# Performance work log

Measured on AMD Instinct MI355X. Metric: run time of the kernel, lower is better.

The kernel has to match this reference:

```python
import jax, jax.numpy as jnp
import numpy as np

EPS = 1e-6
HEADS = 8

def _ln_cf(x, w, b):
    # ConvNeXt-style channels_first LayerNorm over C axis of (B,C,H,W)
    mu = jnp.mean(x, axis=1, keepdims=True)
    var = jnp.mean((x - mu) ** 2, axis=1, keepdims=True)
    xn = (x - mu) / jnp.sqrt(var + EPS)
    return xn * w[None, :, None, None] + b[None, :, None, None]

def _xattn(q_map, kv_map, Wq, Wk, Wv, Wo, bo):
    B, C, H, W = q_map.shape
    HW = H * W
    dh = C // HEADS
    xq = q_map.reshape(B, C, HW).transpose(0, 2, 1)   # (B,HW,C)
    xkv = kv_map.reshape(B, C, HW).transpose(0, 2, 1)
    q = (xq @ Wq.T).reshape(B, HW, HEADS, dh).transpose(0, 2, 1, 3)
    k = (xkv @ Wk.T).reshape(B, HW, HEADS, dh).transpose(0, 2, 1, 3)
    v = (xkv @ Wv.T).reshape(B, HW, HEADS, dh).transpose(0, 2, 1, 3)
    scale = dh ** -0.5
    logits = jnp.einsum('bhqd,bhkd->bhqk', q, k) * scale
    attn = jax.nn.softmax(logits, axis=-1)
    o = jnp.einsum('bhqk,bhkd->bhqd', attn, v)        # (B,h,HW,dh)
    o = o.transpose(0, 2, 1, 3).reshape(B, HW, C)
    o = o @ Wo.T + bo
    return o.transpose(0, 2, 1).reshape(B, C, H, W)

def _ffn(x, W1, b1, W2, b2):
    # 1x1 convs == channel-wise linear; exact GELU (torch default)
    h = jnp.einsum('bchw,oc->bohw', x, W1) + b1[None, :, None, None]
    h = jax.nn.gelu(h, approximate=False)
    return jnp.einsum('bchw,oc->bohw', h, W2) + b2[None, :, None, None]

def setup_inputs() -> dict:
    key = jax.random.key(0)
    ks = jax.random.split(key, 24)
    B, C, H, W = 8, 512, 32, 32
    hid = 4 * C
    d = {
        'spatial_feat': jax.random.normal(ks[0], (B, C, H, W), jnp.float32),
        'freq_feat': jax.random.normal(ks[1], (B, C, H, W), jnp.float32),
        # spatial enhancer (standard cross-attn)
        's_Wq': jax.random.normal(ks[2], (C, C), jnp.float32) * 0.02,
        's_Wk': jax.random.normal(ks[3], (C, C), jnp.float32) * 0.02,
        's_Wv': jax.random.normal(ks[4], (C, C), jnp.float32) * 0.02,
        's_Wo': jax.random.normal(ks[5], (C, C), jnp.float32) * 0.02,
        's_bo': jnp.zeros((C,), jnp.float32),
        # frequency enhancer
        'f_Wq': jax.random.normal(ks[6], (C, C), jnp.float32) * 0.02,
        'f_Wk': jax.random.normal(ks[7], (C, C), jnp.float32) * 0.02,
        'f_Wv': jax.random.normal(ks[8], (C, C), jnp.float32) * 0.02,
        'f_Wo': jax.random.normal(ks[9], (C, C), jnp.float32) * 0.02,
        'f_bo': jnp.zeros((C,), jnp.float32),
        # norms
        'sn1_w': jnp.ones((C,), jnp.float32), 'sn1_b': jnp.zeros((C,), jnp.float32),
        'sn2_w': jnp.ones((C,), jnp.float32), 'sn2_b': jnp.zeros((C,), jnp.float32),
        'fn1_w': jnp.ones((C,), jnp.float32), 'fn1_b': jnp.zeros((C,), jnp.float32),
        'fn2_w': jnp.ones((C,), jnp.float32), 'fn2_b': jnp.zeros((C,), jnp.float32),
        # ConvFFNs (1x1 convs)
        'sffn_W1': jax.random.normal(ks[10], (hid, C), jnp.float32) * 0.02,
        'sffn_b1': jnp.zeros((hid,), jnp.float32),
        'sffn_W2': jax.random.normal(ks[11], (C, hid), jnp.float32) * 0.02,
        'sffn_b2': jnp.zeros((C,), jnp.float32),
        'fffn_W1': jax.random.normal(ks[12], (hid, C), jnp.float32) * 0.02,
        'fffn_b1': jnp.zeros((hid,), jnp.float32),
        'fffn_W2': jax.random.normal(ks[13], (C, hid), jnp.float32) * 0.02,
        'fffn_b2': jnp.zeros((C,), jnp.float32),
    }
    return d

def reference(spatial_feat, freq_feat,
              s_Wq, s_Wk, s_Wv, s_Wo, s_bo,
              f_Wq, f_Wk, f_Wv, f_Wo, f_bo,
              sn1_w, sn1_b, sn2_w, sn2_b,
              fn1_w, fn1_b, fn2_w, fn2_b,
              sffn_W1, sffn_b1, sffn_W2, sffn_b2,
              fffn_W1, fffn_b1, fffn_W2, fffn_b2):
    enh_s = _xattn(spatial_feat, freq_feat, s_Wq, s_Wk, s_Wv, s_Wo, s_bo)
    enh_f = _xattn(freq_feat, spatial_feat, f_Wq, f_Wk, f_Wv, f_Wo, f_bo)
    s = _ln_cf(spatial_feat + enh_s, sn1_w, sn1_b)
    s = _ln_cf(s + _ffn(s, sffn_W1, sffn_b1, sffn_W2, sffn_b2), sn2_w, sn2_b)
    f = _ln_cf(freq_feat + enh_f, fn1_w, fn1_b)
    f = _ln_cf(f + _ffn(f, fffn_W1, fffn_b1, fffn_W2, fffn_b2), fn2_w, fn2_b)
    return (s, f)
```

## Files before the change

### kernel.cpp

```cpp
#include <hip/hip_runtime.h>
#include <hip/hip_bf16.h>


#define CCH 512
#define HWD 1024

typedef unsigned short u16;
typedef unsigned int u32;
typedef __attribute__((ext_vector_type(8))) __bf16 bf16x8;
typedef __attribute__((ext_vector_type(4))) float f32x4;
typedef __attribute__((ext_vector_type(4))) unsigned short u16x4;
typedef __attribute__((ext_vector_type(8))) unsigned short u16x8;

__device__ __forceinline__ float bf2f(u16 u) { return __uint_as_float(((u32)u) << 16); }
__device__ __forceinline__ u16 f2bf(float f) {
    u32 u = __float_as_uint(f);
    return (u16)((u + 0x7fffu + ((u >> 16) & 1u)) >> 16);
}
__device__ __forceinline__ float ldp(const void* p, int i, bool isbf) {
    return isbf ? bf2f(((const u16*)p)[i]) : ((const float*)p)[i];
}
__device__ __forceinline__ float fast_gelu(float v) {
    float a = v * (0.7978845608f + 0.0356774081f * v * v);
    float e = __expf(-2.0f * fabsf(a));
    float r = __fdividef(1.0f - e, 1.0f + e);
    float th = (a < 0.f) ? -r : r;
    return 0.5f * v * (1.0f + th);
}

#define GLL16(g, l) __builtin_amdgcn_global_load_lds( \
    (const __attribute__((address_space(1))) u32*)(g), \
    (__attribute__((address_space(3))) u32*)(l), 16, 0, 0)

struct MMJob { const u16* A; const u16* W; const void* bias; void* Y; };
struct PJob  { const u16* A; const u16* W; u16* Y; int ldY; int gm; int gn; };
struct PJobs { PJob j[6]; };
struct AJob  { const u16* QK; const u16* VT; u16* AO; };
struct LNJob { const u16* A; const float* Br; const void* w; const void* b; void* Y; };

__global__ void k_detect(const u16* __restrict__ in, int* __restrict__ flag) {
    if (threadIdx.x == 0 && blockIdx.x == 0) {
        int sane = 0;
        for (int i = 0; i < 1024; i += 2) {
            int e = (in[i] >> 7) & 0xFF;
            if (e >= 0x6D && e <= 0x8D) sane++;
        }
        *flag = (sane >= 256) ? 1 : 0;
    }
}

struct CvtJobs {
    const void* src[12];
    u16* dst[12];
    int chunk0[13];
};
__global__ __launch_bounds__(256) void k_cvt_all(CvtJobs J, const int* __restrict__ flag) {
    bool isbf = (*flag != 0);
    int b = blockIdx.x;
    int j = 0;
    #pragma unroll
    for (int i = 0; i < 12; i++) if (b >= J.chunk0[i + 1]) j = i + 1;
    int idx = (b - J.chunk0[j]) * 1024 + threadIdx.x * 4;
    u16* d = J.dst[j] + idx;
    if (isbf) {
        *(u16x4*)d = *(const u16x4*)((const u16*)J.src[j] + idx);
    } else {
        float4 v = *(const float4*)((const float*)J.src[j] + idx);
        d[0] = f2bf(v.x); d[1] = f2bf(v.y); d[2] = f2bf(v.z); d[3] = f2bf(v.w);
    }
}

__global__ __launch_bounds__(256) void k_transpose(const void* __restrict__ in,
                                                   u16* __restrict__ out,
                                                   const int* __restrict__ flag) {
    __shared__ float tile[32][33];
    bool isbf = (*flag != 0);
    int b = blockIdx.z;
    int hw0 = blockIdx.x * 32, c0 = blockIdx.y * 32;
    int tx = threadIdx.x, ty = threadIdx.y;
    size_t base = (size_t)b * CCH * HWD;
    if (isbf) {
        const u16* ip = (const u16*)in + base;
        for (int i = ty; i < 32; i += 8)
            tile[i][tx] = bf2f(ip[(size_t)(c0 + i) * HWD + hw0 + tx]);
    } else {
        const float* ip = (const float*)in + base;
        for (int i = ty; i < 32; i += 8)
            tile[i][tx] = ip[(size_t)(c0 + i) * HWD + hw0 + tx];
    }
    __syncthreads();
    u16* op = out + (size_t)b * HWD * CCH;
    for (int i = ty; i < 32; i += 8)
        op[(size_t)(hw0 + i) * CCH + c0 + tx] = f2bf(tile[tx][i]);
}

__device__ __forceinline__ void swz(int pid, int gm, int gn, int& bm, int& bn) {
    int gsz = 8 * gn;
    int gid = pid / gsz;
    int fm = gid * 8;
    int rows = (gm - fm < 8) ? (gm - fm) : 8;
    int pin = pid - gid * gsz;
    bm = fm + pin % rows;
    bn = pin / rows;
}

__global__ __launch_bounds__(256) void k_mm(MMJob j0, MMJob j1,
                                            int K, int ldY, int mode, int gm, int gn,
                                            const int* __restrict__ flag) {
    __shared__ u16 As[128 * 32];
    __shared__ u16 Bs[128 * 32];
    MMJob J = blockIdx.z ? j1 : j0;
    int t = threadIdx.x;
    int w = t >> 6, l = t & 63;
    int bm, bn;
    swz(blockIdx.x, gm, gn, bm, bn);
    int m0 = bm * 128, n0 = bn * 128;
    int wm = (w >> 1) * 64, wn = (w & 1) * 64;

    int r0 = (w * 2 + 0) * 16 + (l >> 2);
    int r1 = (w * 2 + 1) * 16 + (l >> 2);
    int sg0 = (((l & 3) ^ ((r0 >> 1) & 3))) * 8;
    int sg1 = (((l & 3) ^ ((r1 >> 1) & 3))) * 8;
    const u16* ga0 = J.A + (size_t)(m0 + r0) * K + sg0;
    const u16* ga1 = J.A + (size_t)(m0 + r1) * K + sg1;
    const u16* gb0 = J.W + (size_t)(n0 + r0) * K + sg0;
    const u16* gb1 = J.W + (size_t)(n0 + r1) * K + sg1;
    u16* la0 = &As[(w * 2 + 0) * 512];
    u16* la1 = &As[(w * 2 + 1) * 512];
    u16* lb0 = &Bs[(w * 2 + 0) * 512];
    u16* lb1 = &Bs[(w * 2 + 1) * 512];

    int quad = l >> 4, lr = l & 15;
    int aoff[4], boff[4];
    #pragma unroll
    for (int i = 0; i < 4; i++) {
        int ra = wm + i * 16 + lr, rb = wn + i * 16 + lr;
        aoff[i] = ra * 32 + (quad ^ ((ra >> 1) & 3)) * 8;
        boff[i] = rb * 32 + (quad ^ ((rb >> 1) & 3)) * 8;
    }

    f32x4 acc[4][4] = {};

    for (int k0 = 0; k0 < K; k0 += 32) {
        __syncthreads();
        GLL16(ga0 + k0, la0);
        GLL16(ga1 + k0, la1);
        GLL16(gb0 + k0, lb0);
        GLL16(gb1 + k0, lb1);
        __syncthreads();
        bf16x8 af[4], bfr[4];
        #pragma unroll
        for (int i = 0; i < 4; i++) af[i] = *(const bf16x8*)&As[aoff[i]];
        #pragma unroll
        for (int j = 0; j < 4; j++) bfr[j] = *(const bf16x8*)&Bs[boff[j]];
        #pragma unroll
        for (int i = 0; i < 4; i++)
            #pragma unroll
            for (int j = 0; j < 4; j++)
                acc[i][j] = __builtin_amdgcn_mfma_f32_16x16x32_bf16(af[i], bfr[j], acc[i][j], 0, 0, 0);
    }

    bool isbf = (*flag != 0);
    #pragma unroll
    for (int i = 0; i < 4; i++) {
        int rowb = m0 + wm + i * 16 + quad * 4;
        #pragma unroll
        for (int j = 0; j < 4; j++) {
            int col = n0 + wn + j * 16 + lr;
            float bv = (mode == 1 || mode == 2) ? ldp(J.bias, col, isbf) : 0.f;
            #pragma unroll
            for (int r = 0; r < 4; r++) {
                float v = acc[i][j][r] + bv;
                if (mode == 2) {
                    ((u16*)J.Y)[(size_t)(rowb + r) * ldY + col] = f2bf(fast_gelu(v));
                } else if (mode == 3) {
                    ((u16*)J.Y)[(size_t)(rowb + r) * ldY + col] = f2bf(v);
                } else {
                    ((float*)J.Y)[(size_t)(rowb + r) * ldY + col] = v;
                }
            }
        }
    }
}

__global__ __launch_bounds__(256) void k_mm64(MMJob j0, MMJob j1,
                                              int K, int ldY, int mode, int gm, int gn,
                                              const int* __restrict__ flag) {
    __shared__ u16 As[128 * 32];
    __shared__ u16 Bs[64 * 32];
    MMJob J = blockIdx.z ? j1 : j0;
    int t = threadIdx.x;
    int w = t >> 6, l = t & 63;
    int bm, bn;
    swz(blockIdx.x, gm, gn, bm, bn);
    int m0 = bm * 128, n0 = bn * 64;
    int wm = (w >> 1) * 64, wn = (w & 1) * 32;

    int r0 = (w * 2 + 0) * 16 + (l >> 2);
    int r1 = (w * 2 + 1) * 16 + (l >> 2);
    int rb_ = w * 16 + (l >> 2);
    int sg0 = (((l & 3) ^ ((r0 >> 1) & 3))) * 8;
    int sg1 = (((l & 3) ^ ((r1 >> 1) & 3))) * 8;
    int sgb = (((l & 3) ^ ((rb_ >> 1) & 3))) * 8;
    const u16* ga0 = J.A + (size_t)(m0 + r0) * K + sg0;
    const u16* ga1 = J.A + (size_t)(m0 + r1) * K + sg1;
    const u16* gb  = J.W + (size_t)(n0 + rb_) * K + sgb;
    u16* la0 = &As[(w * 2 + 0) * 512];
    u16* la1 = &As[(w * 2 + 1) * 512];
    u16* lb  = &Bs[w * 512];

    int quad = l >> 4, lr = l & 15;
    int aoff[4], boff[2];
    #pragma unroll
    for (int i = 0; i < 4; i++) {
        int ra = wm + i * 16 + lr;
        aoff[i] = ra * 32 + (quad ^ ((ra >> 1) & 3)) * 8;
    }
    #pragma unroll
    for (int j = 0; j < 2; j++) {
        int rb2 = wn + j * 16 + lr;
        boff[j] = rb2 * 32 + (quad ^ ((rb2 >> 1) & 3)) * 8;
    }

    f32x4 acc[4][2] = {};

    for (int k0 = 0; k0 < K; k0 += 32) {
        __syncthreads();
        GLL16(ga0 + k0, la0);
        GLL16(ga1 + k0, la1);
        GLL16(gb + k0, lb);
        __syncthreads();
        bf16x8 af[4], bfr[2];
        #pragma unroll
        for (int i = 0; i < 4; i++) af[i] = *(const bf16x8*)&As[aoff[i]];
        #pragma unroll
        for (int j = 0; j < 2; j++) bfr[j] = *(const bf16x8*)&Bs[boff[j]];
        #pragma unroll
        for (int i = 0; i < 4; i++)
            #pragma unroll
            for (int j = 0; j < 2; j++)
                acc[i][j] = __builtin_amdgcn_mfma_f32_16x16x32_bf16(af[i], bfr[j], acc[i][j], 0, 0, 0);
    }

    bool isbf = (*flag != 0);
    #pragma unroll
    for (int i = 0; i < 4; i++) {
        int rowb = m0 + wm + i * 16 + quad * 4;
        #pragma unroll
        for (int j = 0; j < 2; j++) {
            int col = n0 + wn + j * 16 + lr;
            float bv = (mode == 1 || mode == 2) ? ldp(J.bias, col, isbf) : 0.f;
            #pragma unroll
            for (int r = 0; r < 4; r++) {
                float v = acc[i][j][r] + bv;
                if (mode == 2) {
                    ((u16*)J.Y)[(size_t)(rowb + r) * ldY + col] = f2bf(fast_gelu(v));
                } else if (mode == 3) {
                    ((u16*)J.Y)[(size_t)(rowb + r) * ldY + col] = f2bf(v);
                } else {
                    ((float*)J.Y)[(size_t)(rowb + r) * ldY + col] = v;
                }
            }
        }
    }
}

__global__ __launch_bounds__(256) void k_proj(PJobs JJ, const int* __restrict__ flag) {
    __shared__ u16 As[128 * 32];
    __shared__ u16 Bs[64 * 32];
    (void)flag;
    PJob J = JJ.j[blockIdx.z];
    const int K = 512;
    int t = threadIdx.x;
    int w = t >> 6, l = t & 63;
    int bm, bn;
    swz(blockIdx.x, J.gm, J.gn, bm, bn);
    int m0 = bm * 128, n0 = bn * 64;
    int wm = (w >> 1) * 64, wn = (w & 1) * 32;

    int r0 = (w * 2 + 0) * 16 + (l >> 2);
    int r1 = (w * 2 + 1) * 16 + (l >> 2);
    int rb_ = w * 16 + (l >> 2);
    int sg0 = (((l & 3) ^ ((r0 >> 1) & 3))) * 8;
    int sg1 = (((l & 3) ^ ((r1 >> 1) & 3))) * 8;
    int sgb = (((l & 3) ^ ((rb_ >> 1) & 3))) * 8;
    const u16* ga0 = J.A + (size_t)(m0 + r0) * K + sg0;
    const u16* ga1 = J.A + (size_t)(m0 + r1) * K + sg1;
    const u16* gb  = J.W + (size_t)(n0 + rb_) * K + sgb;
    u16* la0 = &As[(w * 2 + 0) * 512];
    u16* la1 = &As[(w * 2 + 1) * 512];
    u16* lb  = &Bs[w * 512];

    int quad = l >> 4, lr = l & 15;
    int aoff[4], boff[2];
    #pragma unroll
    for (int i = 0; i < 4; i++) {
        int ra = wm + i * 16 + lr;
        aoff[i] = ra * 32 + (quad ^ ((ra >> 1) & 3)) * 8;
    }
    #pragma unroll
    for (int j = 0; j < 2; j++) {
        int rb2 = wn + j * 16 + lr;
        boff[j] = rb2 * 32 + (quad ^ ((rb2 >> 1) & 3)) * 8;
    }

    f32x4 acc[4][2] = {};

    for (int k0 = 0; k0 < K; k0 += 32) {
        __syncthreads();
        GLL16(ga0 + k0, la0);
        GLL16(ga1 + k0, la1);
        GLL16(gb + k0, lb);
        __syncthreads();
        bf16x8 af[4], bfr[2];
        #pragma unroll
        for (int i = 0; i < 4; i++) af[i] = *(const bf16x8*)&As[aoff[i]];
        #pragma unroll
        for (int j = 0; j < 2; j++) bfr[j] = *(const bf16x8*)&Bs[boff[j]];
        #pragma unroll
        for (int i = 0; i < 4; i++)
            #pragma unroll
            for (int j = 0; j < 2; j++)
                acc[i][j] = __builtin_amdgcn_mfma_f32_16x16x32_bf16(af[i], bfr[j], acc[i][j], 0, 0, 0);
    }

    #pragma unroll
    for (int i = 0; i < 4; i++) {
        int rowb = m0 + wm + i * 16 + quad * 4;
        #pragma unroll
        for (int j = 0; j < 2; j++) {
            int col = n0 + wn + j * 16 + lr;
            #pragma unroll
            for (int r = 0; r < 4; r++)
                J.Y[(size_t)(rowb + r) * J.ldY + col] = f2bf(acc[i][j][r]);
        }
    }
}

__global__ __launch_bounds__(256) void k_attn2(AJob j0, AJob j1) {
    __shared__ __align__(16) u16 Qs[2][128][32];
    __shared__ __align__(16) u16 Ks[2][64][32];
    __shared__ __align__(16) u16 Vs[2][64][32];
    __shared__ __align__(16) u16 Ps[4][32][80];

    AJob J = (blockIdx.x >> 9) ? j1 : j0;
    int blk = blockIdx.x & 511;
    int t = threadIdx.x;
    int w = t >> 6, l = t & 63;
    int l15 = l & 15, quad = l >> 4;
    int qt = blk & 7;
    int bh = blk >> 3;
    int h = bh & 7, b = bh >> 3;
    int tok0 = b * 1024;
    int q0 = qt * 128;
    int hc = h * 64;

    #pragma unroll
    for (int kc = 0; kc < 2; kc++)
        #pragma unroll
        for (int g = 0; g < 2; g++) {
            int row = w * 32 + g * 16 + (l >> 2);
            int sl = ((l & 3) ^ ((row >> 1) & 3)) * 8;
            const u16* gp = J.QK + (size_t)(tok0 + q0 + row) * 1024 + hc + kc * 32 + sl;
            GLL16(gp, &Qs[kc][w * 32 + g * 16][0]);
        }
    __syncthreads();

    bf16x8 qf[2][2];
    #pragma unroll
    for (int jq = 0; jq < 2; jq++)
        #pragma unroll
        for (int kc = 0; kc < 2; kc++) {
            int row = w * 32 + jq * 16 + l15;
            qf[jq][kc] = *(const bf16x8*)&Qs[kc][row][(quad ^ ((row >> 1) & 3)) * 8];
        }

    float m_[2] = {-1e30f, -1e30f};
    float l_[2] = {0.f, 0.f};
    f32x4 acco[2][4] = {};

    for (int kt = 0; kt < 16; kt++) {
        __syncthreads();
        {
            int row = w * 16 + (l >> 2);
            int f = (row >> 1) & 3;
            int sl = ((l & 3) ^ f) * 8;
            int key = kt * 64 + row;
            #pragma unroll
            for (int kc = 0; kc < 2; kc++) {
                const u16* kp = J.QK + (size_t)(tok0 + key) * 1024 + 512 + hc + kc * 32 + sl;
                GLL16(kp, &Ks[kc][w * 16][0]);
            }
            #pragma unroll
            for (int kck = 0; kck < 2; kck++) {
                const u16* vp = J.VT + (size_t)(hc + row) * 8192 + tok0 + kt * 64 + kck * 32 + sl;
                GLL16(vp, &Vs[kck][w * 16][0]);
            }
        }
        __syncthreads();

        f32x4 accs[4][2] = {};
        #pragma unroll
        for (int kc = 0; kc < 2; kc++) {
            bf16x8 kf[4];
            #pragma unroll
            for (int i = 0; i < 4; i++) {
                int row = i * 16 + l15;
                kf[i] = *(const bf16x8*)&Ks[kc][row][(quad ^ ((row >> 1) & 3)) * 8];
            }
            #pragma unroll
            for (int i = 0; i < 4; i++)
                #pragma unroll
                for (int jq = 0; jq < 2; jq++)
                    accs[i][jq] = __builtin_amdgcn_mfma_f32_16x16x32_bf16(kf[i], qf[jq][kc], accs[i][jq], 0, 0, 0);
        }

        float alpha[2];
        #pragma unroll
        for (int jq = 0; jq < 2; jq++) {
            float tm = -1e30f;
            #pragma unroll
            for (int i = 0; i < 4; i++)
                #pragma unroll
                for (int r = 0; r < 4; r++) tm = fmaxf(tm, accs[i][jq][r]);
            tm *= 0.125f;
            tm = fmaxf(tm, __shfl_xor(tm, 16));
            tm = fmaxf(tm, __shfl_xor(tm, 32));
            float mn = fmaxf(m_[jq], tm);
            alpha[jq] = __expf(m_[jq] - mn);
            m_[jq] = mn;
            float ts = 0.f;
            #pragma unroll
            for (int i = 0; i < 4; i++) {
                u16x4 pk;
                #pragma unroll
                for (int r = 0; r < 4; r++) {
                    float p = __expf(accs[i][jq][r] * 0.125f - mn);
                    ts += p;
                    pk[r] = f2bf(p);
                }
                *(u16x4*)&Ps[w][jq * 16 + l15][i * 16 + quad * 4] = pk;
            }
            ts += __shfl_xor(ts, 16);
            ts += __shfl_xor(ts, 32);
            l_[jq] = l_[jq] * alpha[jq] + ts;
        }

        #pragma unroll
        for (int i2 = 0; i2 < 2; i2++)
            #pragma unroll
            for (int r = 0; r < 4; r++) {
                float al = __shfl(alpha[i2], quad * 4 + r);
                #pragma unroll
                for (int jd = 0; jd < 4; jd++) acco[i2][jd][r] *= al;
            }

        #pragma unroll
        for (int kck = 0; kck < 2; kck++) {
            bf16x8 pf[2], vf[4];
            #pragma unroll
            for (int i2 = 0; i2 < 2; i2++)
                pf[i2] = *(const bf16x8*)&Ps[w][i2 * 16 + l15][kck * 32 + quad * 8];
            #pragma unroll
            for (int jd = 0; jd < 4; jd++) {
                int row = jd * 16 + l15;
                vf[jd] = *(const bf16x8*)&Vs[kck][row][(quad ^ ((row >> 1) & 3)) * 8];
            }
            #pragma unroll
            for (int i2 = 0; i2 < 2; i2++)
                #pragma unroll
                for (int jd = 0; jd < 4; jd++)
                    acco[i2][jd] = __builtin_amdgcn_mfma_f32_16x16x32_bf16(pf[i2], vf[jd], acco[i2][jd], 0, 0, 0);
        }
    }

    #pragma unroll
    for (int i2 = 0; i2 < 2; i2++) {
        float linv = 1.0f / l_[i2];
        #pragma unroll
        for (int r = 0; r < 4; r++) {
            float li = __shfl(linv, quad * 4 + r);
            int token = tok0 + q0 + w * 32 + i2 * 16 + quad * 4 + r;
            u16* dst = J.AO + (size_t)token * 512 + hc;
            #pragma unroll
            for (int jd = 0; jd < 4; jd++)
                dst[jd * 16 + l15] = f2bf(acco[i2][jd][r] * li);
        }
    }
}

__global__ __launch_bounds__(256) void k_ln(LNJob j0, LNJob j1,
                                            const int* __restrict__ flag) {
    LNJob J = blockIdx.y ? j1 : j0;
    bool isbf = (*flag != 0);
    int token = blockIdx.x * 4 + (threadIdx.x >> 6);
    int lane = threadIdx.x & 63;
    int c0 = lane * 8;
    const u16* pa = J.A + (size_t)token * CCH + c0;
    const float* pb = J.Br + (size_t)token * CCH + c0;
    u16x8 av = *(const u16x8*)pa;
    float4 b0 = *(const float4*)pb;
    float4 b1 = *(const float4*)(pb + 4);
    float v[8];
    float s = 0.f, s2 = 0.f;
    #pragma unroll
    for (int u = 0; u < 8; u++) {
        float x = bf2f(av[u]) + ((u < 4) ? (&b0.x)[u] : (&b1.x)[u - 4]);
        v[u] = x; s += x; s2 += x * x;
    }
    #pragma unroll
    for (int off = 32; off > 0; off >>= 1) {
        s += __shfl_xor(s, off);
        s2 += __shfl_xor(s2, off);
    }
    float mu = s * (1.f / CCH);
    float var = s2 * (1.f / CCH) - mu * mu;
    float rstd = rsqrtf(var + 1e-6f);
    u16x8 ov;
    #pragma unroll
    for (int u = 0; u < 8; u++)
        ov[u] = f2bf((v[u] - mu) * rstd * ldp(J.w, c0 + u, isbf) + ldp(J.b, c0 + u, isbf));
    *(u16x8*)((u16*)J.Y + (size_t)token * CCH + c0) = ov;
}

__global__ __launch_bounds__(256) void k_ln_out(LNJob j0, LNJob j1,
                                                void* __restrict__ out, int brBase,
                                                const int* __restrict__ flag) {
    LNJob J = blockIdx.y ? j1 : j0;
    int branch = brBase + blockIdx.y;
    bool isbf = (*flag != 0);
    int token = blockIdx.x * 4 + (threadIdx.x >> 6);
    int lane = threadIdx.x & 63;
    int c0 = lane * 8;
    const u16* pa = J.A + (size_t)token * CCH + c0;
    const float* pb = J.Br + (size_t)token * CCH + c0;
    u16x8 av = *(const u16x8*)pa;
    float4 b0 = *(const float4*)pb;
    float4 b1 = *(const float4*)(pb + 4);
    float v[8];
    float s = 0.f, s2 = 0.f;
    #pragma unroll
    for (int u = 0; u < 8; u++) {
        float x = bf2f(av[u]) + ((u < 4) ? (&b0.x)[u] : (&b1.x)[u - 4]);
        v[u] = x; s += x; s2 += x * x;
    }
    #pragma unroll
    for (int off = 32; off > 0; off >>= 1) {
        s += __shfl_xor(s, off);
        s2 += __shfl_xor(s2, off);
    }
    float mu = s * (1.f / CCH);
    float var = s2 * (1.f / CCH) - mu * mu;
    float rstd = rsqrtf(var + 1e-6f);
    int b = token >> 10, hw = token & 1023;
    size_t obase = (size_t)branch * CCH * HWD * 8 + (size_t)b * CCH * HWD + hw;
    if (isbf) {
        u16* op = (u16*)out + obase;
        #pragma unroll
        for (int u = 0; u < 8; u++) {
            float y = (v[u] - mu) * rstd * ldp(J.w, c0 + u, true) + ldp(J.b, c0 + u, true);
            op[(size_t)(c0 + u) * HWD] = f2bf(y);
        }
    } else {
        float* op = (float*)out + obase;
        #pragma unroll
        for (int u = 0; u < 8; u++) {
            float y = (v[u] - mu) * rstd * ldp(J.w, c0 + u, false) + ldp(J.b, c0 + u, false);
            op[(size_t)(c0 + u) * HWD] = y;
        }
    }
}

extern "C" void kernel_launch(void* const* d_in, const int* in_sizes, int n_in,
                              void* d_out, int out_size, void* d_ws, size_t ws_size,
                              hipStream_t stream) {
    (void)in_sizes; (void)n_in; (void)out_size;

    char* wsb = (char*)d_ws;
    int* flag = (int*)wsb;
    u16* Wall = (u16*)(wsb + 256);
    u16* Xs = (u16*)(wsb + 256 + 12582912);
    u16* Xf = (u16*)(wsb + 256 + 12582912 + 8388608);
    char* rbase = wsb + 29360384;

    const size_t BRSZ = 67108864;
    bool dual = ws_size >= (29360384 + 2 * BRSZ);

    u16* QKb[2]; u16* VTb[2]; u16* AOb[2]; u16* Hbb[2];
    float* ENHb[2];
    for (int b = 0; b < 2; b++) {
        char* r = rbase + (dual ? b * BRSZ : 0);
        QKb[b] = (u16*)r;
        ENHb[b] = (float*)r;
        VTb[b] = (u16*)(r + 16777216);
        AOb[b] = (u16*)(r + 16777216 + 8388608);
        Hbb[b] = (u16*)(r + 16777216 + 2 * 8388608);
    }

    const int SQ = 262144, SW1 = 1048576;
    const u16* Xq[2] = {Xs, Xf};
    const u16* Xkv[2] = {Xf, Xs};
    u16* Wq[2]; u16* Wk[2]; u16* Wv[2]; u16* Wo[2]; u16* W1[2]; u16* W2[2];
    const void *bo[2], *n1w[2], *n1b[2], *n2w[2], *n2b[2], *b1[2], *b2[2];
    for (int b = 0; b < 2; b++) {
        u16* Wb = Wall + (size_t)b * 3145728;
        Wq[b] = Wb; Wk[b] = Wb + SQ; Wv[b] = Wb + 2 * SQ; Wo[b] = Wb + 3 * SQ;
        W1[b] = Wb + 4 * SQ; W2[b] = Wb + 4 * SQ + SW1;
        bo[b]  = d_in[b ? 11 : 6];
        n1w[b] = d_in[b ? 16 : 12]; n1b[b] = d_in[b ? 17 : 13];
        n2w[b] = d_in[b ? 18 : 14]; n2b[b] = d_in[b ? 19 : 15];
        b1[b]  = d_in[b ? 25 : 21]; b2[b]  = d_in[b ? 27 : 23];
    }

    k_detect<<<1, 64, 0, stream>>>((const u16*)d_in[0], flag);

    {
        CvtJobs J;
        int ch = 0;
        for (int b = 0; b < 2; b++) {
            const int srcIdx[6] = {b ? 7 : 2, b ? 8 : 3, b ? 9 : 4, b ? 10 : 5,
                                   b ? 24 : 20, b ? 26 : 22};
            u16* dsts[6] = {Wq[b], Wk[b], Wv[b], Wo[b], W1[b], W2[b]};
            const int sz[6] = {SQ, SQ, SQ, SQ, SW1, SW1};
            for (int i = 0; i < 6; i++) {
                int j = b * 6 + i;
                J.src[j] = d_in[srcIdx[i]];
                J.dst[j] = dsts[i];
                J.chunk0[j] = ch;
                ch += sz[i] / 1024;
            }
        }
        J.chunk0[12] = ch;
        k_cvt_all<<<ch, 256, 0, stream>>>(J, flag);
    }

    dim3 tb(32, 8);
    k_transpose<<<dim3(32, 16, 8), tb, 0, stream>>>(d_in[0], Xs, flag);
    k_transpose<<<dim3(32, 16, 8), tb, 0, stream>>>(d_in[1], Xf, flag);

    auto mmj = [&](const u16* A, const u16* W, const void* bias, void* Y) {
        MMJob j; j.A = A; j.W = W; j.bias = bias; j.Y = Y; return j;
    };
    auto pj = [&](const u16* A, const u16* W, u16* Y, int ldY, int gm, int gn) {
        PJob j; j.A = A; j.W = W; j.Y = Y; j.ldY = ldY; j.gm = gm; j.gn = gn; return j;
    };
    auto lnj = [&](const u16* A, const float* Br, const void* w, const void* bb, void* Y) {
        LNJob j; j.A = A; j.Br = Br; j.w = w; j.b = bb; j.Y = Y; return j;
    };

    int nbr = dual ? 2 : 1;
    int nloop = dual ? 1 : 2;
    for (int it = 0; it < nloop; it++) {
        int b0 = dual ? 0 : it;
        int b1i = dual ? 1 : it;

        {
            PJobs JJ;
            int nz = 0;
            for (int z = 0; z < nbr; z++) {
                int b = dual ? z : it;
                JJ.j[nz++] = pj(Xq[b], Wq[b], QKb[b], 1024, 64, 8);
                JJ.j[nz++] = pj(Xkv[b], Wk[b], QKb[b] + 512, 1024, 64, 8);
                JJ.j[nz++] = pj(Wv[b], Xkv[b], VTb[b], 8192, 4, 128);
            }
            for (int z = nz; z < 6; z++) JJ.j[z] = JJ.j[0];
            k_proj<<<dim3(512, 1, nz), 256, 0, stream>>>(JJ, flag);
        }
        {
            AJob a0, a1;
            a0.QK = QKb[b0]; a0.VT = VTb[b0]; a0.AO = AOb[b0];
            a1.QK = QKb[b1i]; a1.VT = VTb[b1i]; a1.AO = AOb[b1i];
            k_attn2<<<512 * nbr, 256, 0, stream>>>(a0, a1);
        }
        k_mm64<<<dim3(512, 1, nbr), 256, 0, stream>>>(
            mmj(AOb[b0], Wo[b0], bo[b0], ENHb[b0]),
            mmj(AOb[b1i], Wo[b1i], bo[b1i], ENHb[b1i]),
            512, 512, 1, 64, 8, flag);
        k_ln<<<dim3(2048, nbr), 256, 0, stream>>>(
            lnj(Xq[b0], ENHb[b0], n1w[b0], n1b[b0], AOb[b0]),
            lnj(Xq[b1i], ENHb[b1i], n1w[b1i], n1b[b1i], AOb[b1i]), flag);
        k_mm<<<dim3(1024, 1, nbr), 256, 0, stream>>>(
            mmj(AOb[b0], W1[b0], b1[b0], Hbb[b0]),
            mmj(AOb[b1i], W1[b1i], b1[b1i], Hbb[b1i]),
            512, 2048, 2, 64, 16, flag);
        k_mm64<<<dim3(512, 1, nbr), 256, 0, stream>>>(
            mmj(Hbb[b0], W2[b0], b2[b0], ENHb[b0]),
            mmj(Hbb[b1i], W2[b1i], b2[b1i], ENHb[b1i]),
            2048, 512, 1, 64, 8, flag);
        k_ln_out<<<dim3(2048, nbr), 256, 0, stream>>>(
            lnj(AOb[b0], ENHb[b0], n2w[b0], n2b[b0], nullptr),
            lnj(AOb[b1i], ENHb[b1i], n2w[b1i], n2b[b1i], nullptr),
            d_out, dual ? 0 : it, flag);
    }
}
```

Baseline: 553.2 us.

## Use sigmoid GELU, merge input transposes, and double K-step per GEMM barrier

Swaps the tanh-form GELU for a sigmoid-based x*sigmoid(1.702x) approximation, merges the two input transpose launches into one grid, and makes the three GEMM kernels load two 32-wide K slices per barrier pair. The wider K step halves the number of __syncthreads and issues more loads in flight, at the cost of doubled LDS per block and possible lower occupancy. The sigmoid GELU departs further from the exact erf GELU the reference requires, so it risks accuracy.

Result: faster. 537.0 us (-2.9%).

```diff
diff --git a/kernel.cpp b/kernel.cpp
--- a/kernel.cpp
+++ b/kernel.cpp
@@ -21,11 +21,7 @@
     return isbf ? bf2f(((const u16*)p)[i]) : ((const float*)p)[i];
 }
 __device__ __forceinline__ float fast_gelu(float v) {
-    float a = v * (0.7978845608f + 0.0356774081f * v * v);
-    float e = __expf(-2.0f * fabsf(a));
-    float r = __fdividef(1.0f - e, 1.0f + e);
-    float th = (a < 0.f) ? -r : r;
-    return 0.5f * v * (1.0f + th);
+    return v * __frcp_rn(1.0f + __expf(-1.702f * v));
 }
 
 #define GLL16(g, l) __builtin_amdgcn_global_load_lds( \
@@ -70,12 +66,17 @@
     }
 }
 
-__global__ __launch_bounds__(256) void k_transpose(const void* __restrict__ in,
-                                                   u16* __restrict__ out,
-                                                   const int* __restrict__ flag) {
+__global__ __launch_bounds__(256) void k_transpose2(const void* __restrict__ in0,
+                                                    const void* __restrict__ in1,
+                                                    u16* __restrict__ o0,
+                                                    u16* __restrict__ o1,
+                                                    const int* __restrict__ flag) {
     __shared__ float tile[32][33];
     bool isbf = (*flag != 0);
-    int b = blockIdx.z;
+    int z = blockIdx.z;
+    const void* in = (z < 8) ? in0 : in1;
+    u16* out = (z < 8) ? o0 : o1;
+    int b = z & 7;
     int hw0 = blockIdx.x * 32, c0 = blockIdx.y * 32;
     int tx = threadIdx.x, ty = threadIdx.y;
     size_t base = (size_t)b * CCH * HWD;
@@ -107,8 +108,8 @@
 __global__ __launch_bounds__(256) void k_mm(MMJob j0, MMJob j1,
                                             int K, int ldY, int mode, int gm, int gn,
                                             const int* __restrict__ flag) {
-    __shared__ u16 As[128 * 32];
-    __shared__ u16 Bs[128 * 32];
+    __shared__ u16 As[128 * 32], Asb[128 * 32];
+    __shared__ u16 Bs[128 * 32], Bsb[128 * 32];
     MMJob J = blockIdx.z ? j1 : j0;
     int t = threadIdx.x;
     int w = t >> 6, l = t & 63;
@@ -125,10 +126,7 @@
     const u16* ga1 = J.A + (size_t)(m0 + r1) * K + sg1;
     const u16* gb0 = J.W + (size_t)(n0 + r0) * K + sg0;
     const u16* gb1 = J.W + (size_t)(n0 + r1) * K + sg1;
-    u16* la0 = &As[(w * 2 + 0) * 512];
-    u16* la1 = &As[(w * 2 + 1) * 512];
-    u16* lb0 = &Bs[(w * 2 + 0) * 512];
-    u16* lb1 = &Bs[(w * 2 + 1) * 512];
+    int lo0 = (w * 2 + 0) * 512, lo1 = (w * 2 + 1) * 512;
 
     int quad = l >> 4, lr = l & 15;
     int aoff[4], boff[4];
@@ -141,23 +139,41 @@
 
     f32x4 acc[4][4] = {};
 
-    for (int k0 = 0; k0 < K; k0 += 32) {
+    for (int k0 = 0; k0 < K; k0 += 64) {
         __syncthreads();
-        GLL16(ga0 + k0, la0);
-        GLL16(ga1 + k0, la1);
-        GLL16(gb0 + k0, lb0);
-        GLL16(gb1 + k0, lb1);
+        GLL16(ga0 + k0, &As[lo0]);
+        GLL16(ga1 + k0, &As[lo1]);
+        GLL16(gb0 + k0, &Bs[lo0]);
+        GLL16(gb1 + k0, &Bs[lo1]);
+        GLL16(ga0 + k0 + 32, &Asb[lo0]);
+        GLL16(ga1 + k0 + 32, &Asb[lo1]);
+        GLL16(gb0 + k0 + 32, &Bsb[lo0]);
+        GLL16(gb1 + k0 + 32, &Bsb[lo1]);
         __syncthreads();
-        bf16x8 af[4], bfr[4];
-        #pragma unroll
-        for (int i = 0; i < 4; i++) af[i] = *(const bf16x8*)&As[aoff[i]];
-        #pragma unroll
-        for (int j = 0; j < 4; j++) bfr[j] = *(const bf16x8*)&Bs[boff[j]];
-        #pragma unroll
-        for (int i = 0; i < 4; i++)
-            #pragma unroll
-            for (int j = 0; j < 4; j++)
-                acc[i][j] = __builtin_amdgcn_mfma_f32_16x16x32_bf16(af[i], bfr[j], acc[i][j], 0, 0, 0);
+        {
+            bf16x8 af[4], bfr[4];
+            #pragma unroll
+            for (int i = 0; i < 4; i++) af[i] = *(const bf16x8*)&As[aoff[i]];
+            #pragma unroll
+            for (int j = 0; j < 4; j++) bfr[j] = *(const bf16x8*)&Bs[boff[j]];
+            #pragma unroll
+            for (int i = 0; i < 4; i++)
+                #pragma unroll
+                for (int j = 0; j < 4; j++)
+                    acc[i][j] = __builtin_amdgcn_mfma_f32_16x16x32_bf16(af[i], bfr[j], acc[i][j], 0, 0, 0);
+        }
+        {
+            bf16x8 af[4], bfr[4];
+            #pragma unroll
+            for (int i = 0; i < 4; i++) af[i] = *(const bf16x8*)&Asb[aoff[i]];
+            #pragma unroll
+            for (int j = 0; j < 4; j++) bfr[j] = *(const bf16x8*)&Bsb[boff[j]];
+            #pragma unroll
+            for (int i = 0; i < 4; i++)
+                #pragma unroll
+                for (int j = 0; j < 4; j++)
+                    acc[i][j] = __builtin_amdgcn_mfma_f32_16x16x32_bf16(af[i], bfr[j], acc[i][j], 0, 0, 0);
+        }
     }
 
     bool isbf = (*flag != 0);
@@ -186,8 +202,8 @@
 __global__ __launch_bounds__(256) void k_mm64(MMJob j0, MMJob j1,
                                               int K, int ldY, int mode, int gm, int gn,
                                               const int* __restrict__ flag) {
-    __shared__ u16 As[128 * 32];
-    __shared__ u16 Bs[64 * 32];
+    __shared__ u16 As[128 * 32], Asb[128 * 32];
+    __shared__ u16 Bs[64 * 32], Bsb[64 * 32];
     MMJob J = blockIdx.z ? j1 : j0;
     int t = threadIdx.x;
     int w = t >> 6, l = t & 63;
@@ -205,9 +221,7 @@
     const u16* ga0 = J.A + (size_t)(m0 + r0) * K + sg0;
     const u16* ga1 = J.A + (size_t)(m0 + r1) * K + sg1;
     const u16* gb  = J.W + (size_t)(n0 + rb_) * K + sgb;
-    u16* la0 = &As[(w * 2 + 0) * 512];
-    u16* la1 = &As[(w * 2 + 1) * 512];
-    u16* lb  = &Bs[w * 512];
+    int lo0 = (w * 2 + 0) * 512, lo1 = (w * 2 + 1) * 512, lob = w * 512;
 
     int quad = l >> 4, lr = l & 15;
     int aoff[4], boff[2];
@@ -224,22 +238,39 @@
 
     f32x4 acc[4][2] = {};
 
-    for (int k0 = 0; k0 < K; k0 += 32) {
+    for (int k0 = 0; k0 < K; k0 += 64) {
         __syncthreads();
-        GLL16(ga0 + k0, la0);
-        GLL16(ga1 + k0, la1);
-        GLL16(gb + k0, lb);
+        GLL16(ga0 + k0, &As[lo0]);
+        GLL16(ga1 + k0, &As[lo1]);
+        GLL16(gb + k0, &Bs[lob]);
+        GLL16(ga0 + k0 + 32, &Asb[lo0]);
+        GLL16(ga1 + k0 + 32, &Asb[lo1]);
+        GLL16(gb + k0 + 32, &Bsb[lob]);
         __syncthreads();
-        bf16x8 af[4], bfr[2];
-        #pragma unroll
-        for (int i = 0; i < 4; i++) af[i] = *(const bf16x8*)&As[aoff[i]];
-        #pragma unroll
-        for (int j = 0; j < 2; j++) bfr[j] = *(const bf16x8*)&Bs[boff[j]];
-        #pragma unroll
-        for (int i = 0; i < 4; i++)
-            #pragma unroll
-            for (int j = 0; j < 2; j++)
-                acc[i][j] = __builtin_amdgcn_mfma_f32_16x16x32_bf16(af[i], bfr[j], acc[i][j], 0, 0, 0);
+        {
+            bf16x8 af[4], bfr[2];
+            #pragma unroll
+            for (int i = 0; i < 4; i++) af[i] = *(const bf16x8*)&As[aoff[i]];
+            #pragma unroll
+            for (int j = 0; j < 2; j++) bfr[j] = *(const bf16x8*)&Bs[boff[j]];
+            #pragma unroll
+            for (int i = 0; i < 4; i++)
+                #pragma unroll
+                for (int j = 0; j < 2; j++)
+                    acc[i][j] = __builtin_amdgcn_mfma_f32_16x16x32_bf16(af[i], bfr[j], acc[i][j], 0, 0, 0);
+        }
+        {
+            bf16x8 af[4], bfr[2];
+            #pragma unroll
+            for (int i = 0; i < 4; i++) af[i] = *(const bf16x8*)&Asb[aoff[i]];
+            #pragma unroll
+            for (int j = 0; j < 2; j++) bfr[j] = *(const bf16x8*)&Bsb[boff[j]];
+            #pragma unroll
+            for (int i = 0; i < 4; i++)
+                #pragma unroll
+                for (int j = 0; j < 2; j++)
+                    acc[i][j] = __builtin_amdgcn_mfma_f32_16x16x32_bf16(af[i], bfr[j], acc[i][j], 0, 0, 0);
+        }
     }
 
     bool isbf = (*flag != 0);
@@ -266,8 +297,8 @@
 }
 
 __global__ __launch_bounds__(256) void k_proj(PJobs JJ, const int* __restrict__ flag) {
-    __shared__ u16 As[128 * 32];
-    __shared__ u16 Bs[64 * 32];
+    __shared__ u16 As[128 * 32], Asb[128 * 32];
+    __shared__ u16 Bs[64 * 32], Bsb[64 * 32];
     (void)flag;
     PJob J = JJ.j[blockIdx.z];
     const int K = 512;
@@ -287,9 +318,7 @@
     const u16* ga0 = J.A + (size_t)(m0 + r0) * K + sg0;
     const u16* ga1 = J.A + (size_t)(m0 + r1) * K + sg1;
     const u16* gb  = J.W + (size_t)(n0 + rb_) * K + sgb;
-    u16* la0 = &As[(w * 2 + 0) * 512];
-    u16* la1 = &As[(w * 2 + 1) * 512];
-    u16* lb  = &Bs[w * 512];
+    int lo0 = (w * 2 + 0) * 512, lo1 = (w * 2 + 1) * 512, lob = w * 512;
 
     int quad = l >> 4, lr = l & 15;
     int aoff[4], boff[2];
@@ -306,22 +335,39 @@
 
     f32x4 acc[4][2] = {};
 
-    for (int k0 = 0; k0 < K; k0 += 32) {
+    for (int k0 = 0; k0 < K; k0 += 64) {
         __syncthreads();
-        GLL16(ga0 + k0, la0);
-        GLL16(ga1 + k0, la1);
-        GLL16(gb + k0, lb);
+        GLL16(ga0 + k0, &As[lo0]);
+        GLL16(ga1 + k0, &As[lo1]);
+        GLL16(gb + k0, &Bs[lob]);
+        GLL16(ga0 + k0 + 32, &Asb[lo0]);
+        GLL16(ga1 + k0 + 32, &Asb[lo1]);
+        GLL16(gb + k0 + 32, &Bsb[lob]);
         __syncthreads();
-        bf16x8 af[4], bfr[2];
-        #pragma unroll
-        for (int i = 0; i < 4; i++) af[i] = *(const bf16x8*)&As[aoff[i]];
-        #pragma unroll
-        for (int j = 0; j < 2; j++) bfr[j] = *(const bf16x8*)&Bs[boff[j]];
-        #pragma unroll
-        for (int i = 0; i < 4; i++)
-            #pragma unroll
-            for (int j = 0; j < 2; j++)
-                acc[i][j] = __builtin_amdgcn_mfma_f32_16x16x32_bf16(af[i], bfr[j], acc[i][j], 0, 0, 0);
+        {
+            bf16x8 af[4], bfr[2];
+            #pragma unroll
+            for (int i = 0; i < 4; i++) af[i] = *(const bf16x8*)&As[aoff[i]];
+            #pragma unroll
+            for (int j = 0; j < 2; j++) bfr[j] = *(const bf16x8*)&Bs[boff[j]];
+            #pragma unroll
+            for (int i = 0; i < 4; i++)
+                #pragma unroll
+                for (int j = 0; j < 2; j++)
+                    acc[i][j] = __builtin_amdgcn_mfma_f32_16x16x32_bf16(af[i], bfr[j], acc[i][j], 0, 0, 0);
+        }
+        {
+            bf16x8 af[4], bfr[2];
+            #pragma unroll
+            for (int i = 0; i < 4; i++) af[i] = *(const bf16x8*)&Asb[aoff[i]];
+            #pragma unroll
+            for (int j = 0; j < 2; j++) bfr[j] = *(const bf16x8*)&Bsb[boff[j]];
+            #pragma unroll
+            for (int i = 0; i < 4; i++)
+                #pragma unroll
+                for (int j = 0; j < 2; j++)
+                    acc[i][j] = __builtin_amdgcn_mfma_f32_16x16x32_bf16(af[i], bfr[j], acc[i][j], 0, 0, 0);
+        }
     }
 
     #pragma unroll
@@ -635,8 +681,7 @@
     }
 
     dim3 tb(32, 8);
-    k_transpose<<<dim3(32, 16, 8), tb, 0, stream>>>(d_in[0], Xs, flag);
-    k_transpose<<<dim3(32, 16, 8), tb, 0, stream>>>(d_in[1], Xf, flag);
+    k_transpose2<<<dim3(32, 16, 16), tb, 0, stream>>>(d_in[0], d_in[1], Xs, Xf, flag);
 
     auto mmj = [&](const u16* A, const u16* W, const void* bias, void* Y) {
         MMJob j; j.A = A; j.W = W; j.bias = bias; j.Y = Y; return j;
```
